# Kernel tuning notes

Measured on AMD Instinct MI355X. Metric: run time of the kernel, lower is better.

The kernel has to match this reference:

```python
import jax, jax.numpy as jnp
import numpy as np

# OpenCV fixed separable Gaussian kernel for ksize=3, sigma=0 (getGaussianKernel small-kernel table)
GAUSS_1D = jnp.array([0.25, 0.5, 0.25], dtype=jnp.float32)
# OpenCV Laplacian kernel for ksize=3 (Sobel dxx + dyy aperture 3)
LAP_K = jnp.array([[2.0, 0.0, 2.0], [0.0, -8.0, 0.0], [2.0, 0.0, 2.0]], dtype=jnp.float32)


def _depthwise_conv(img, kernel2d):
    # img: (N, H, W); kernel2d: (kh, kw). BORDER_REFLECT_101 == jnp.pad mode='reflect'.
    kh, kw = kernel2d.shape
    ph, pw = kh // 2, kw // 2
    padded = jnp.pad(img, ((0, 0), (ph, ph), (pw, pw)), mode='reflect')
    out = jax.lax.conv_general_dilated(
        padded[:, None, :, :], kernel2d[None, None, :, :],
        window_strides=(1, 1), padding='VALID')
    return out[:, 0]


def setup_inputs() -> dict:
    key = jax.random.key(0)
    x = jax.random.uniform(key, (32, 3, 512, 512), dtype=jnp.float32)
    return {"x": x}


def reference(x):
    B, C, H, W = x.shape
    img = x.reshape(B * C, H, W)
    # src = clip(x*255, 0, 255).astype('uint8')  -> truncation toward zero (values >= 0, so floor)
    src = jnp.floor(jnp.clip(img * 255.0, 0.0, 255.0))
    # cv2.GaussianBlur(ksize=3, sigma=0): separable [1,2,1]/4 kernel, rounded back to uint8
    g2d = GAUSS_1D[:, None] * GAUSS_1D[None, :]
    blurred = jnp.clip(jnp.round(_depthwise_conv(src, g2d)), 0.0, 255.0)
    # cv2.Laplacian(CV_16S, ksize=3): integer-exact on integer-valued input
    lap = _depthwise_conv(blurred, LAP_K)
    # cv2.convertScaleAbs: saturate_cast<uchar>(|dst|)
    abs_dst = jnp.clip(jnp.round(jnp.abs(lap)), 0.0, 255.0)
    return abs_dst.reshape(B, C, H, W)
```

## Files before the change

### kernel.cpp

```cpp
#include <hip/hip_runtime.h>
#include <math.h>

#define IMG_H 512
#define IMG_W 512
#define TW 256
#define TH 32
#define SRC_ROWS 36
#define SRC_SLOTS 66

__device__ __forceinline__ int reflect101(int i, int n) {
    if (i < 0) i = -i;
    if (i >= n) i = 2 * n - 2 - i;
    return i;
}

__device__ __forceinline__ unsigned int quant(float v) {
    return (unsigned int)floorf(fminf(fmaxf(v * 255.0f, 0.0f), 255.0f));
}

__device__ __forceinline__ void unpack_row(const unsigned int* __restrict__ row, int cx,
                                           float f[8]) {
    unsigned int u0 = row[cx], u1 = row[cx + 1], u2 = row[cx + 2];
    f[0] = (float)((u0 >> 16) & 0xffu);
    f[1] = (float)((u0 >> 24) & 0xffu);
    f[2] = (float)(u1 & 0xffu);
    f[3] = (float)((u1 >> 8) & 0xffu);
    f[4] = (float)((u1 >> 16) & 0xffu);
    f[5] = (float)((u1 >> 24) & 0xffu);
    f[6] = (float)(u2 & 0xffu);
    f[7] = (float)((u2 >> 8) & 0xffu);
}

__device__ __forceinline__ void blur_row(const float a[8], const float b[8], const float c[8],
                                         float bl[6]) {
    float cs[8];
    #pragma unroll
    for (int j = 0; j < 8; ++j) cs[j] = a[j] + 2.0f * b[j] + c[j];
    #pragma unroll
    for (int j = 0; j < 6; ++j)
        bl[j] = rintf((cs[j] + 2.0f * cs[j + 1] + cs[j + 2]) * 0.0625f);
}

__global__ __launch_bounds__(256, 4) void lap_fused(const float* __restrict__ in,
                                                    float* __restrict__ out) {
    __shared__ unsigned int s_src[SRC_ROWS][SRC_SLOTS];

    const int img = blockIdx.z;
    const int ty0 = blockIdx.y * TH;
    const int tx0 = blockIdx.x * TW;
    const float* __restrict__ ip = in + (size_t)img * (IMG_H * IMG_W);
    float* __restrict__ op = out + (size_t)img * (IMG_H * IMG_W);
    const int tid = threadIdx.x;

    for (int i = tid; i < SRC_ROWS * SRC_SLOTS; i += 256) {
        int r = i / SRC_SLOTS;
        int j = i - r * SRC_SLOTS;
        int gy = reflect101(ty0 + r - 2, IMG_H);
        int gx0 = tx0 - 4 + 4 * j;
        const float* rowp = ip + (size_t)gy * IMG_W;
        float4 v;
        if (gx0 >= 0 && gx0 + 3 < IMG_W) {
            v = *(const float4*)(rowp + gx0);
        } else {
            float* pv = (float*)&v;
            #pragma unroll
            for (int k = 0; k < 4; ++k) pv[k] = rowp[reflect101(gx0 + k, IMG_W)];
        }
        unsigned int p = quant(v.x) | (quant(v.y) << 8) | (quant(v.z) << 16) | (quant(v.w) << 24);
        s_src[r][j] = p;
    }
    __syncthreads();

    const int cx = tid & 63;
    const int rw = tid >> 6;
    const int xo = tx0 + 4 * cx;
    const int lr0 = 8 * rw;

    float s[3][8];
    unpack_row(&s_src[lr0 + 0][0], cx, s[0]);
    unpack_row(&s_src[lr0 + 1][0], cx, s[1]);
    unpack_row(&s_src[lr0 + 2][0], cx, s[2]);
    float bl[3][6];
    blur_row(s[0], s[1], s[2], bl[0]);
    unpack_row(&s_src[lr0 + 3][0], cx, s[0]);
    blur_row(s[1], s[2], s[0], bl[1]);

    #pragma unroll
    for (int k = 0; k < 8; ++k) {
        unpack_row(&s_src[lr0 + 4 + k][0], cx, s[(k + 1) % 3]);
        blur_row(s[(k + 2) % 3], s[k % 3], s[(k + 1) % 3], bl[(k + 2) % 3]);

        const float* bm1 = bl[k % 3];
        const float* b0  = bl[(k + 1) % 3];
        const float* bp1 = bl[(k + 2) % 3];
        float4 o;
        float* po = (float*)&o;
        #pragma unroll
        for (int d = 0; d < 4; ++d) {
            float h = (bm1[d] + bm1[d + 2] + bp1[d] + bp1[d + 2]) - 4.0f * b0[d + 1];
            po[d] = fminf(2.0f * fabsf(h), 255.0f);
        }
        *(float4*)&op[(size_t)(ty0 + 8 * rw + k) * IMG_W + xo] = o;
    }
}

extern "C" void kernel_launch(void* const* d_in, const int* in_sizes, int n_in,
                              void* d_out, int out_size, void* d_ws, size_t ws_size,
                              hipStream_t stream) {
    const float* x = (const float*)d_in[0];
    float* out = (float*)d_out;
    dim3 grid(IMG_W / TW, IMG_H / TH, 96);
    dim3 block(256);
    lap_fused<<<grid, block, 0, stream>>>(x, out);
}
```

Baseline: 46.22 us.

## Double per-thread output width, halve block size, split border loads from interior

Each thread now computes an 8x8 output patch instead of 4x8 with 128-thread blocks, reusing vertical partial sums across rows via register rotation. The shared-memory fill separates the unguarded interior float4 loads from the reflect-handled edge slots, and quantisation drops the clamp/floor in favour of a direct integer cast. This aims to cut LDS traffic and ALU redundancy per output, at the cost of higher register pressure and fewer threads to hide memory latency. The unclamped cast relies on inputs lying in [0,1).

```diff
diff --git a/kernel.cpp b/kernel.cpp
--- a/kernel.cpp
+++ b/kernel.cpp
@@ -8,40 +8,94 @@
 #define SRC_ROWS 36
 #define SRC_SLOTS 66
 
+typedef float f32x4 __attribute__((ext_vector_type(4)));
+
 __device__ __forceinline__ int reflect101(int i, int n) {
     if (i < 0) i = -i;
     if (i >= n) i = 2 * n - 2 - i;
     return i;
 }
 
-__device__ __forceinline__ unsigned int quant(float v) {
-    return (unsigned int)floorf(fminf(fmaxf(v * 255.0f, 0.0f), 255.0f));
+__device__ __forceinline__ unsigned int quant4(float4 v) {
+    unsigned int a = (unsigned int)(v.x * 255.0f);
+    unsigned int b = (unsigned int)(v.y * 255.0f);
+    unsigned int c = (unsigned int)(v.z * 255.0f);
+    unsigned int d = (unsigned int)(v.w * 255.0f);
+    return a | (b << 8) | (c << 16) | (d << 24);
 }
 
-__device__ __forceinline__ void unpack_row(const unsigned int* __restrict__ row, int cx,
-                                           float f[8]) {
-    unsigned int u0 = row[cx], u1 = row[cx + 1], u2 = row[cx + 2];
-    f[0] = (float)((u0 >> 16) & 0xffu);
-    f[1] = (float)((u0 >> 24) & 0xffu);
-    f[2] = (float)(u1 & 0xffu);
-    f[3] = (float)((u1 >> 8) & 0xffu);
-    f[4] = (float)((u1 >> 16) & 0xffu);
-    f[5] = (float)((u1 >> 24) & 0xffu);
-    f[6] = (float)(u2 & 0xffu);
-    f[7] = (float)((u2 >> 8) & 0xffu);
-}
+#define LOADR(k, RA, RB) do {                                                 \
+    RA = *(const uint2*)&s_src[lr0 + (k)][sb];                                \
+    RB = *(const uint2*)&s_src[lr0 + (k)][sb + 2];                            \
+} while (0)
 
-__device__ __forceinline__ void blur_row(const float a[8], const float b[8], const float c[8],
-                                         float bl[6]) {
-    float cs[8];
-    #pragma unroll
-    for (int j = 0; j < 8; ++j) cs[j] = a[j] + 2.0f * b[j] + c[j];
-    #pragma unroll
-    for (int j = 0; j < 6; ++j)
-        bl[j] = rintf((cs[j] + 2.0f * cs[j + 1] + cs[j + 2]) * 0.0625f);
-}
+#define UNPK(RA, RB, Q) do {                                                  \
+    Q##0  = (float)((RA.x >> 16) & 0xffu);                                    \
+    Q##1  = (float)(RA.x >> 24);                                              \
+    Q##2  = (float)(RA.y & 0xffu);                                            \
+    Q##3  = (float)((RA.y >> 8) & 0xffu);                                     \
+    Q##4  = (float)((RA.y >> 16) & 0xffu);                                    \
+    Q##5  = (float)(RA.y >> 24);                                              \
+    Q##6  = (float)(RB.x & 0xffu);                                            \
+    Q##7  = (float)((RB.x >> 8) & 0xffu);                                     \
+    Q##8  = (float)((RB.x >> 16) & 0xffu);                                    \
+    Q##9  = (float)(RB.x >> 24);                                              \
+    Q##10 = (float)(RB.y & 0xffu);                                            \
+    Q##11 = (float)((RB.y >> 8) & 0xffu);                                     \
+} while (0)
 
-__global__ __launch_bounds__(256, 4) void lap_fused(const float* __restrict__ in,
+#define EMAKE(E, QA, QB) do {                                                 \
+    E##0 = QA##0 + QB##0;   E##1 = QA##1 + QB##1;                             \
+    E##2 = QA##2 + QB##2;   E##3 = QA##3 + QB##3;                             \
+    E##4 = QA##4 + QB##4;   E##5 = QA##5 + QB##5;                             \
+    E##6 = QA##6 + QB##6;   E##7 = QA##7 + QB##7;                             \
+    E##8 = QA##8 + QB##8;   E##9 = QA##9 + QB##9;                             \
+    E##10 = QA##10 + QB##10; E##11 = QA##11 + QB##11;                         \
+} while (0)
+
+#define BLMAKE(BL, EA, EB) do {                                               \
+    float cs0 = EA##0 + EB##0,   cs1 = EA##1 + EB##1;                         \
+    float cs2 = EA##2 + EB##2,   cs3 = EA##3 + EB##3;                         \
+    float cs4 = EA##4 + EB##4,   cs5 = EA##5 + EB##5;                         \
+    float cs6 = EA##6 + EB##6,   cs7 = EA##7 + EB##7;                         \
+    float cs8 = EA##8 + EB##8,   cs9 = EA##9 + EB##9;                         \
+    float cs10 = EA##10 + EB##10, cs11 = EA##11 + EB##11;                     \
+    float d0 = cs0 + cs1, d1 = cs1 + cs2, d2 = cs2 + cs3, d3 = cs3 + cs4;     \
+    float d4 = cs4 + cs5, d5 = cs5 + cs6, d6 = cs6 + cs7, d7 = cs7 + cs8;     \
+    float d8 = cs8 + cs9, d9 = cs9 + cs10, d10 = cs10 + cs11;                 \
+    BL##0 = rintf((d0 + d1) * 0.0625f);                                       \
+    BL##1 = rintf((d1 + d2) * 0.0625f);                                       \
+    BL##2 = rintf((d2 + d3) * 0.0625f);                                       \
+    BL##3 = rintf((d3 + d4) * 0.0625f);                                       \
+    BL##4 = rintf((d4 + d5) * 0.0625f);                                       \
+    BL##5 = rintf((d5 + d6) * 0.0625f);                                       \
+    BL##6 = rintf((d6 + d7) * 0.0625f);                                       \
+    BL##7 = rintf((d7 + d8) * 0.0625f);                                       \
+    BL##8 = rintf((d8 + d9) * 0.0625f);                                       \
+    BL##9 = rintf((d9 + d10) * 0.0625f);                                      \
+} while (0)
+
+#define OUTROW(BA, BB, BC, T) do {                                            \
+    float u0 = BA##0 + BC##0, u1 = BA##1 + BC##1, u2 = BA##2 + BC##2;         \
+    float u3 = BA##3 + BC##3, u4 = BA##4 + BC##4, u5 = BA##5 + BC##5;         \
+    float u6 = BA##6 + BC##6, u7 = BA##7 + BC##7, u8 = BA##8 + BC##8;         \
+    float u9 = BA##9 + BC##9;                                                 \
+    f32x4 oA_, oB_;                                                           \
+    float h_;                                                                 \
+    h_ = fmaf(-4.0f, BB##1, u0 + u2); oA_.x = fminf(2.0f * fabsf(h_), 255.0f);\
+    h_ = fmaf(-4.0f, BB##2, u1 + u3); oA_.y = fminf(2.0f * fabsf(h_), 255.0f);\
+    h_ = fmaf(-4.0f, BB##3, u2 + u4); oA_.z = fminf(2.0f * fabsf(h_), 255.0f);\
+    h_ = fmaf(-4.0f, BB##4, u3 + u5); oA_.w = fminf(2.0f * fabsf(h_), 255.0f);\
+    h_ = fmaf(-4.0f, BB##5, u4 + u6); oB_.x = fminf(2.0f * fabsf(h_), 255.0f);\
+    h_ = fmaf(-4.0f, BB##6, u5 + u7); oB_.y = fminf(2.0f * fabsf(h_), 255.0f);\
+    h_ = fmaf(-4.0f, BB##7, u6 + u8); oB_.z = fminf(2.0f * fabsf(h_), 255.0f);\
+    h_ = fmaf(-4.0f, BB##8, u7 + u9); oB_.w = fminf(2.0f * fabsf(h_), 255.0f);\
+    float* orow_ = &op[(size_t)(ty0 + yb + (T)) * IMG_W + xo];                \
+    *(f32x4*)orow_ = oA_;                                                     \
+    *(f32x4*)(orow_ + 4) = oB_;                                               \
+} while (0)
+
+__global__ __launch_bounds__(128, 4) void lap_fused(const float* __restrict__ in,
                                                     float* __restrict__ out) {
     __shared__ unsigned int s_src[SRC_ROWS][SRC_SLOTS];
 
@@ -52,56 +106,80 @@
     float* __restrict__ op = out + (size_t)img * (IMG_H * IMG_W);
     const int tid = threadIdx.x;
 
-    for (int i = tid; i < SRC_ROWS * SRC_SLOTS; i += 256) {
-        int r = i / SRC_SLOTS;
-        int j = i - r * SRC_SLOTS;
+    {
+        const int j = 1 + (tid & 63);
+        const int r0 = tid >> 6;
+        const int gx0 = tx0 - 4 + 4 * j;
+        #pragma unroll
+        for (int k = 0; k < 18; ++k) {
+            int r = r0 + 2 * k;
+            int gy = reflect101(ty0 + r - 2, IMG_H);
+            float4 v = *(const float4*)(ip + (size_t)gy * IMG_W + gx0);
+            s_src[r][j] = quant4(v);
+        }
+    }
+    if (tid < 72) {
+        int r = tid >> 1;
+        int j = (tid & 1) * 65;
         int gy = reflect101(ty0 + r - 2, IMG_H);
         int gx0 = tx0 - 4 + 4 * j;
         const float* rowp = ip + (size_t)gy * IMG_W;
         float4 v;
-        if (gx0 >= 0 && gx0 + 3 < IMG_W) {
-            v = *(const float4*)(rowp + gx0);
-        } else {
-            float* pv = (float*)&v;
-            #pragma unroll
-            for (int k = 0; k < 4; ++k) pv[k] = rowp[reflect101(gx0 + k, IMG_W)];
-        }
-        unsigned int p = quant(v.x) | (quant(v.y) << 8) | (quant(v.z) << 16) | (quant(v.w) << 24);
-        s_src[r][j] = p;
+        float* pv = (float*)&v;
+        #pragma unroll
+        for (int k = 0; k < 4; ++k) pv[k] = rowp[reflect101(gx0 + k, IMG_W)];
+        s_src[r][j] = quant4(v);
     }
     __syncthreads();
 
-    const int cx = tid & 63;
-    const int rw = tid >> 6;
-    const int xo = tx0 + 4 * cx;
-    const int lr0 = 8 * rw;
+    const int cg = tid & 31;
+    const int rb = tid >> 5;
+    const int xo = tx0 + 8 * cg;
+    const int sb = 2 * cg;
+    const int lr0 = 8 * rb;
+    const int yb = 8 * rb;
 
-    float s[3][8];
-    unpack_row(&s_src[lr0 + 0][0], cx, s[0]);
-    unpack_row(&s_src[lr0 + 1][0], cx, s[1]);
-    unpack_row(&s_src[lr0 + 2][0], cx, s[2]);
-    float bl[3][6];
-    blur_row(s[0], s[1], s[2], bl[0]);
-    unpack_row(&s_src[lr0 + 3][0], cx, s[0]);
-    blur_row(s[1], s[2], s[0], bl[1]);
+    uint2 r0a, r0b, r1a, r1b, r2a, r2b, r3a, r3b, r4a, r4b, r5a, r5b;
+    uint2 r6a, r6b, r7a, r7b, r8a, r8b, r9a, r9b, r10a, r10b, r11a, r11b;
+    float qA0, qA1, qA2, qA3, qA4, qA5, qA6, qA7, qA8, qA9, qA10, qA11;
+    float qB0, qB1, qB2, qB3, qB4, qB5, qB6, qB7, qB8, qB9, qB10, qB11;
+    float eA0, eA1, eA2, eA3, eA4, eA5, eA6, eA7, eA8, eA9, eA10, eA11;
+    float eB0, eB1, eB2, eB3, eB4, eB5, eB6, eB7, eB8, eB9, eB10, eB11;
+    float bP0, bP1, bP2, bP3, bP4, bP5, bP6, bP7, bP8, bP9;
+    float bQ0, bQ1, bQ2, bQ3, bQ4, bQ5, bQ6, bQ7, bQ8, bQ9;
+    float bR0, bR1, bR2, bR3, bR4, bR5, bR6, bR7, bR8, bR9;
 
-    #pragma unroll
-    for (int k = 0; k < 8; ++k) {
-        unpack_row(&s_src[lr0 + 4 + k][0], cx, s[(k + 1) % 3]);
-        blur_row(s[(k + 2) % 3], s[k % 3], s[(k + 1) % 3], bl[(k + 2) % 3]);
-
-        const float* bm1 = bl[k % 3];
-        const float* b0  = bl[(k + 1) % 3];
-        const float* bp1 = bl[(k + 2) % 3];
-        float4 o;
-        float* po = (float*)&o;
-        #pragma unroll
-        for (int d = 0; d < 4; ++d) {
-            float h = (bm1[d] + bm1[d + 2] + bp1[d] + bp1[d + 2]) - 4.0f * b0[d + 1];
-            po[d] = fminf(2.0f * fabsf(h), 255.0f);
-        }
-        *(float4*)&op[(size_t)(ty0 + 8 * rw + k) * IMG_W + xo] = o;
-    }
+    LOADR(0, r0a, r0b); LOADR(1, r1a, r1b); LOADR(2, r2a, r2b); LOADR(3, r3a, r3b);
+    UNPK(r0a, r0b, qA);
+    UNPK(r1a, r1b, qB);  EMAKE(eA, qA, qB);
+    LOADR(4, r4a, r4b);
+    UNPK(r2a, r2b, qA);  EMAKE(eB, qB, qA);
+    BLMAKE(bP, eA, eB);
+    LOADR(5, r5a, r5b);
+    UNPK(r3a, r3b, qB);  EMAKE(eA, qA, qB);
+    BLMAKE(bQ, eB, eA);
+    LOADR(6, r6a, r6b);
+    UNPK(r4a, r4b, qA);  EMAKE(eB, qB, qA);  BLMAKE(bR, eA, eB);
+    OUTROW(bP, bQ, bR, 0);
+    LOADR(7, r7a, r7b);
+    UNPK(r5a, r5b, qB);  EMAKE(eA, qA, qB);  BLMAKE(bP, eB, eA);
+    OUTROW(bQ, bR, bP, 1);
+    LOADR(8, r8a, r8b);
+    UNPK(r6a, r6b, qA);  EMAKE(eB, qB, qA);  BLMAKE(bQ, eA, eB);
+    OUTROW(bR, bP, bQ, 2);
+    LOADR(9, r9a, r9b);
+    UNPK(r7a, r7b, qB);  EMAKE(eA, qA, qB);  BLMAKE(bR, eB, eA);
+    OUTROW(bP, bQ, bR, 3);
+    LOADR(10, r10a, r10b);
+    UNPK(r8a, r8b, qA);  EMAKE(eB, qB, qA);  BLMAKE(bP, eA, eB);
+    OUTROW(bQ, bR, bP, 4);
+    LOADR(11, r11a, r11b);
+    UNPK(r9a, r9b, qB);  EMAKE(eA, qA, qB);  BLMAKE(bQ, eB, eA);
+    OUTROW(bR, bP, bQ, 5);
+    UNPK(r10a, r10b, qA); EMAKE(eB, qB, qA); BLMAKE(bR, eA, eB);
+    OUTROW(bP, bQ, bR, 6);
+    UNPK(r11a, r11b, qB); EMAKE(eA, qA, qB); BLMAKE(bP, eB, eA);
+    OUTROW(bQ, bR, bP, 7);
 }
 
 extern "C" void kernel_launch(void* const* d_in, const int* in_sizes, int n_in,
@@ -110,6 +188,6 @@
     const float* x = (const float*)d_in[0];
     float* out = (float*)d_out;
     dim3 grid(IMG_W / TW, IMG_H / TH, 96);
-    dim3 block(256);
+    dim3 block(128);
     lap_fused<<<grid, block, 0, stream>>>(x, out);
 }
```

Measured after the change: 40.26 us. 12.9% less time.
